# Kernel tuning notes

Hardware: AMD Instinct MI355X
Metric: run time of the kernel (lower is better)

Reference implementation:

```python
import jax, jax.numpy as jnp
import numpy as np

B, L, D_MODEL, H, D_K, D_V = 64, 52, 4096, 32, 128, 128
NEW_C = D_MODEL // H  # per-head input channel after the (faithful) raw reshape


def setup_inputs() -> dict:
    key = jax.random.key(0)
    ks = jax.random.split(key, 12)
    s = 0.02
    return {
        "Q": jax.random.normal(ks[0], (B, L, D_MODEL), jnp.float32),
        "K": jax.random.normal(ks[1], (B, L, D_MODEL), jnp.float32),
        "V": jax.random.normal(ks[2], (B, L, D_MODEL), jnp.float32),
        "Wq": jax.random.normal(ks[3], (H, NEW_C, D_K), jnp.float32) * s,
        "bq": jnp.zeros((H, D_K), jnp.float32),
        "Wk": jax.random.normal(ks[4], (H, NEW_C, D_K), jnp.float32) * s,
        "bk": jnp.zeros((H, D_K), jnp.float32),
        "Wv": jax.random.normal(ks[5], (H, NEW_C, D_V), jnp.float32) * s,
        "bv": jnp.zeros((H, D_V), jnp.float32),
        "Wo": jax.random.normal(ks[6], (H * D_V, D_MODEL), jnp.float32) * s,
        "bo": jnp.zeros((D_MODEL,), jnp.float32),
    }


def reference(Q, K, V, Wq, bq, Wk, bk, Wv, bv, Wo, bo):
    # Faithful to source: raw reshape (B, L, D) -> (B, H, L, D/H), NOT a channel split.
    def split(x):
        return x.reshape(B, H, L, NEW_C)

    q = jnp.einsum('bhlc,hck->bhlk', split(Q), Wq) + bq[None, :, None, :]  # (B,H,L,D_K)
    k = jnp.einsum('bhlc,hck->bhlk', split(K), Wk) + bk[None, :, None, :]
    v = jnp.einsum('bhlc,hcv->bhlv', split(V), Wv) + bv[None, :, None, :]

    scores = jnp.einsum('bhqk,bhmk->bhqm', q, k) / jnp.sqrt(jnp.asarray(D_K, q.dtype))
    # causal mask: keep j <= i, else -inf (matches the numpy masking loop)
    causal = jnp.tril(jnp.ones((L, L), bool))
    scores = jnp.where(causal[None, None], scores, -jnp.inf)
    attn = jax.nn.softmax(scores, axis=-1)
    o = jnp.einsum('bhqm,bhmv->bhqv', attn, v)  # (B,H,L,D_V)
    o = o.transpose(0, 2, 1, 3).reshape(B, L, H * D_V)  # concat heads on last axis
    # Dropout(0.1) is identity at inference.
    return o @ Wo + bo
```

## Files before the change

### kernel.cpp

```cpp
#include <hip/hip_runtime.h>
#include <hip/hip_bf16.h>

#define B_SZ   64
#define L_SZ   52
#define DMODEL 4096
#define H_SZ   32
#define C_SZ   128
#define DK     128

#define GM 3328
#define GN 4096
#define GK 4096

typedef __bf16 bf16x8 __attribute__((ext_vector_type(8)));
typedef float  f32x4  __attribute__((ext_vector_type(4)));

__device__ __forceinline__ void gload_lds16(const void* g, void* l) {
  __builtin_amdgcn_global_load_lds(
      (__attribute__((address_space(1))) void*)(void*)g,
      (__attribute__((address_space(3))) void*)l, 16, 0, 0);
}

__device__ __forceinline__ unsigned short bfbits(float x) {
  union { __hip_bfloat16 h; unsigned short u; } c;
  c.h = __float2bfloat16(x);
  return c.u;
}

__device__ __forceinline__ int hwoff(int row, int g) {
  return row * 128 + ((g ^ (row & 7)) << 3);
}
__device__ __forceinline__ int wdoff(int row, int g) {
  return row * 64 + ((g ^ (row & 7)) << 2);
}

__global__ __launch_bounds__(256) void w3_transpose_kernel(
    const float* __restrict__ Wq, const float* __restrict__ Wk,
    const float* __restrict__ Wv, __hip_bfloat16* __restrict__ WqT,
    __hip_bfloat16* __restrict__ WkT, __hip_bfloat16* __restrict__ WvT) {
  __shared__ float tile[64][65];
  const int bz = blockIdx.z;
  const float* in = (bz < 32 ? Wq : (bz < 64 ? Wk : Wv)) + (size_t)(bz & 31) * 16384;
  __hip_bfloat16* out = (bz < 32 ? WqT : (bz < 64 ? WkT : WvT)) + (size_t)(bz & 31) * 16384;
  const int nt = blockIdx.x, mt = blockIdx.y;
  const int t = threadIdx.x;
  const int r  = t >> 4;
  const int c4 = (t & 15) << 2;
#pragma unroll
  for (int p = 0; p < 4; ++p) {
    const int rr = r + p * 16;
    const float4 v = *(const float4*)(in + (size_t)(mt * 64 + rr) * 128 + nt * 64 + c4);
    tile[rr][c4 + 0] = v.x; tile[rr][c4 + 1] = v.y;
    tile[rr][c4 + 2] = v.z; tile[rr][c4 + 3] = v.w;
  }
  __syncthreads();
#pragma unroll
  for (int p = 0; p < 4; ++p) {
    const int rr = r + p * 16;
    union { __hip_bfloat16 h[4]; ushort4 u; } o4;
#pragma unroll
    for (int e = 0; e < 4; ++e) o4.h[e] = __float2bfloat16(tile[c4 + e][rr]);
    *(ushort4*)(out + (size_t)(nt * 64 + rr) * 128 + mt * 64 + c4) = o4.u;
  }
}

__device__ __forceinline__ void proj_swz(
    const __hip_bfloat16* __restrict__ xs, const __hip_bfloat16* __restrict__ WT,
    const float* __restrict__ bias, __hip_bfloat16* __restrict__ out,
    int n0, int r16, int kq) {
  f32x4 acc[2][4] = {};
  bf16x8 wf[2][4];
#pragma unroll
  for (int ct = 0; ct < 2; ++ct)
#pragma unroll
    for (int kk = 0; kk < 4; ++kk)
      wf[ct][kk] = *(const bf16x8*)(WT + (n0 + ct * 16 + r16) * 128 + kk * 32 + kq * 8);
#pragma unroll
  for (int kk = 0; kk < 4; ++kk) {
    bf16x8 xf[4];
#pragma unroll
    for (int rt = 0; rt < 4; ++rt) {
      const int row = rt * 16 + r16;
      const int rowc = row < 52 ? row : 51;
      xf[rt] = *(const bf16x8*)(xs + hwoff(rowc, 4 * kk + kq));
    }
#pragma unroll
    for (int ct = 0; ct < 2; ++ct)
#pragma unroll
      for (int rt = 0; rt < 4; ++rt)
        acc[ct][rt] = __builtin_amdgcn_mfma_f32_16x16x32_bf16(wf[ct][kk], xf[rt], acc[ct][rt], 0, 0, 0);
  }
#pragma unroll
  for (int ct = 0; ct < 2; ++ct) {
    const int col0 = n0 + ct * 16 + kq * 4;
    const float4 b4 = *(const float4*)(bias + col0);
    const int g = (n0 >> 3) + ct * 2 + (kq >> 1);
#pragma unroll
    for (int rt = 0; rt < 4; ++rt) {
      const int row = rt * 16 + r16;
      if (row < 52) {
        ushort4 o;
        o.x = bfbits(acc[ct][rt][0] + b4.x);
        o.y = bfbits(acc[ct][rt][1] + b4.y);
        o.z = bfbits(acc[ct][rt][2] + b4.z);
        o.w = bfbits(acc[ct][rt][3] + b4.w);
        *(ushort4*)(out + hwoff(row, g) + (kq & 1) * 4) = o;
      }
    }
  }
}

__device__ __forceinline__ uint2 shfl64(uint2 v, int lane) {
  uint2 r;
  r.x = (unsigned)__shfl((int)v.x, lane);
  r.y = (unsigned)__shfl((int)v.y, lane);
  return r;
}

__global__ __launch_bounds__(256, 4) void attn_fused_kernel(
    const float* __restrict__ Qin, const float* __restrict__ Kin,
    const float* __restrict__ Vin,
    const __hip_bfloat16* __restrict__ WqT, const float* __restrict__ bq,
    const __hip_bfloat16* __restrict__ WkT, const float* __restrict__ bk,
    const __hip_bfloat16* __restrict__ WvT, const float* __restrict__ bv,
    __hip_bfloat16* __restrict__ Oc,
    const float* __restrict__ Wo, __hip_bfloat16* __restrict__ WoT) {
  __shared__ __align__(16) char lds[39936];
  const int gid = blockIdx.x;
  const int t = threadIdx.x;

  if (gid >= 2048) {
    float* tile = (float*)lds;
    const int bid2 = gid - 2048;
    const int nt = bid2 & 63, mt = bid2 >> 6;
    const int r  = t >> 4;
    const int c4 = (t & 15) << 2;
#pragma unroll
    for (int p = 0; p < 4; ++p) {
      const int rr = r + p * 16;
      const float4 v = *(const float4*)(Wo + (size_t)(mt * 64 + rr) * 4096 + nt * 64 + c4);
      tile[rr * 65 + c4 + 0] = v.x; tile[rr * 65 + c4 + 1] = v.y;
      tile[rr * 65 + c4 + 2] = v.z; tile[rr * 65 + c4 + 3] = v.w;
    }
    __syncthreads();
#pragma unroll
    for (int p = 0; p < 4; ++p) {
      const int rr = r + p * 16;
      union { __hip_bfloat16 h[4]; ushort4 u; } o4;
#pragma unroll
      for (int e = 0; e < 4; ++e) o4.h[e] = __float2bfloat16(tile[(c4 + e) * 65 + rr]);
      *(ushort4*)(WoT + (size_t)(nt * 64 + rr) * 4096 + mt * 64 + c4) = o4.u;
    }
    return;
  }

  __hip_bfloat16* r0 = (__hip_bfloat16*)(lds);
  __hip_bfloat16* r1 = (__hip_bfloat16*)(lds + 13312);
  __hip_bfloat16* r2 = (__hip_bfloat16*)(lds + 26624);
  float*          s_sh = (float*)(lds + 13312);
  __hip_bfloat16* p_sh = r0;

  const int h = gid & 31, bb = gid >> 5;
  const int lane = t & 63;
  const int w = t >> 6;
  const int r16 = lane & 15, kq = lane >> 4;
  const size_t xoff = (size_t)bb * (L_SZ * DMODEL) + (size_t)h * (L_SZ * C_SZ);
  const int n0 = w * 32;

  {
    const float* xp[3] = {Qin + xoff, Kin + xoff, Vin + xoff};
    __hip_bfloat16* xd[3] = {r0, r1, r2};
#pragma unroll
    for (int tz = 0; tz < 3; ++tz) {
      const float* X = xp[tz];
      __hip_bfloat16* xs = xd[tz];
      for (int idx = t; idx < 52 * 32; idx += 256) {
        const int row = idx >> 5, c4 = (idx & 31) << 2;
        const float4 v = *(const float4*)(X + row * 128 + c4);
        union { __hip_bfloat16 h[4]; ushort4 u; } o4;
        o4.h[0] = __float2bfloat16(v.x); o4.h[1] = __float2bfloat16(v.y);
        o4.h[2] = __float2bfloat16(v.z); o4.h[3] = __float2bfloat16(v.w);
        *(ushort4*)(xs + hwoff(row, c4 >> 3) + (c4 & 4)) = o4.u;
      }
    }
  }
  __syncthreads();

  uint2 vb[4][2];
  {
    f32x4 acc[4][2] = {};
    bf16x8 wf[2][4];
    const __hip_bfloat16* WT = WvT + (size_t)h * 16384;
#pragma unroll
    for (int ct = 0; ct < 2; ++ct)
#pragma unroll
      for (int kk = 0; kk < 4; ++kk)
        wf[ct][kk] = *(const bf16x8*)(WT + (n0 + ct * 16 + r16) * 128 + kk * 32 + kq * 8);
#pragma unroll
    for (int kk = 0; kk < 4; ++kk) {
      bf16x8 a[4];
#pragma unroll
      for (int mt = 0; mt < 4; ++mt) {
        const int row = mt * 16 + r16;
        const int rowc = row < 52 ? row : 51;
        a[mt] = *(const bf16x8*)(r2 + hwoff(rowc, 4 * kk + kq));
      }
#pragma unroll
      for (int mt = 0; mt < 4; ++mt)
#pragma unroll
        for (int ct = 0; ct < 2; ++ct)
          acc[mt][ct] = __builtin_amdgcn_mfma_f32_16x16x32_bf16(a[mt], wf[ct][kk], acc[mt][ct], 0, 0, 0);
    }
#pragma unroll
    for (int ct = 0; ct < 2; ++ct) {
      const float bvv = bv[h * 128 + n0 + ct * 16 + r16];
#pragma unroll
      for (int mt = 0; mt < 4; ++mt) {
        vb[mt][ct].x = (unsigned)bfbits(acc[mt][ct][0] + bvv) |
                       ((unsigned)bfbits(acc[mt][ct][1] + bvv) << 16);
        vb[mt][ct].y = (unsigned)bfbits(acc[mt][ct][2] + bvv) |
                       ((unsigned)bfbits(acc[mt][ct][3] + bvv) << 16);
      }
    }
  }
  __syncthreads();

  proj_swz(r0, WqT + (size_t)h * 16384, bq + h * 128, r2, n0, r16, kq);
  __syncthreads();

  proj_swz(r1, WkT + (size_t)h * 16384, bk + h * 128, r0, n0, r16, kq);
  __syncthreads();

  {
    const int nq = w * 16;
    f32x4 sacc[4] = {};
#pragma unroll
    for (int kk = 0; kk < 4; ++kk) {
      const int krow = nq + r16;
      const int krc = krow < 52 ? krow : 51;
      const bf16x8 kf = *(const bf16x8*)(r0 + hwoff(krc, 4 * kk + kq));
#pragma unroll
      for (int mt = 0; mt < 4; ++mt) {
        const int qrow = mt * 16 + r16;
        const int qrc = qrow < 52 ? qrow : 51;
        const bf16x8 a = *(const bf16x8*)(r2 + hwoff(qrc, 4 * kk + kq));
        sacc[mt] = __builtin_amdgcn_mfma_f32_16x16x32_bf16(a, kf, sacc[mt], 0, 0, 0);
      }
    }
    const float scale = 0.08838834764831845f;
    const int c = nq + r16;
#pragma unroll
    for (int mt = 0; mt < 4; ++mt)
#pragma unroll
      for (int i = 0; i < 4; ++i) {
        const int row = mt * 16 + kq * 4 + i;
        if (row < 52) s_sh[wdoff(row, c >> 2) + (c & 3)] = sacc[mt][i] * scale;
      }
  }
  __syncthreads();

  {
    const int r = t >> 2, qd = t & 3;
    if (r < 52) {
      float v[16];
      float mx = -3e38f;
#pragma unroll
      for (int j4 = 0; j4 < 4; ++j4) {
        const f32x4 s4 = *(const f32x4*)(s_sh + wdoff(r, qd * 4 + j4));
#pragma unroll
        for (int e = 0; e < 4; ++e) {
          const int col = qd * 16 + j4 * 4 + e;
          const float val = (col <= r) ? s4[e] : -3e38f;
          v[j4 * 4 + e] = val;
          mx = fmaxf(mx, val);
        }
      }
      mx = fmaxf(mx, __shfl_xor(mx, 1));
      mx = fmaxf(mx, __shfl_xor(mx, 2));
      float ex[16];
      float sum = 0.f;
#pragma unroll
      for (int j = 0; j < 16; ++j) {
        const int col = qd * 16 + j;
        const float e = (col <= r) ? __expf(v[j] - mx) : 0.f;
        ex[j] = e; sum += e;
      }
      sum += __shfl_xor(sum, 1);
      sum += __shfl_xor(sum, 2);
      const float inv = 1.0f / sum;
      union { __hip_bfloat16 h[8]; uint4 q; } p0, p1;
#pragma unroll
      for (int j = 0; j < 8; ++j) {
        p0.h[j] = __float2bfloat16(ex[j] * inv);
        p1.h[j] = __float2bfloat16(ex[8 + j] * inv);
      }
      *(uint4*)(p_sh + hwoff(r, qd * 2))     = p0.q;
      *(uint4*)(p_sh + hwoff(r, qd * 2 + 1)) = p1.q;
    }
  }
  __syncthreads();

  {
    const int half = (kq >> 1) & 1;
    const int src0 = ((kq & 1) << 5) + r16;
    const int src1 = src0 + 16;
    f32x4 oaccT[2][4] = {};
#pragma unroll
    for (int kk = 0; kk < 2; ++kk) {
      bf16x8 bfr[2];
#pragma unroll
      for (int ct = 0; ct < 2; ++ct) {
        const uint2 a0 = shfl64(vb[2 * kk + 0][ct], src0);
        const uint2 a1 = shfl64(vb[2 * kk + 1][ct], src0);
        const uint2 b0 = shfl64(vb[2 * kk + 0][ct], src1);
        const uint2 b1 = shfl64(vb[2 * kk + 1][ct], src1);
        union { unsigned u[4]; bf16x8 v; } asm_;
        asm_.u[0] = half ? a1.x : a0.x;
        asm_.u[1] = half ? a1.y : a0.y;
        asm_.u[2] = half ? b1.x : b0.x;
        asm_.u[3] = half ? b1.y : b0.y;
        bfr[ct] = asm_.v;
      }
      bf16x8 pf[4];
#pragma unroll
      for (int rt = 0; rt < 4; ++rt) {
        const int prow = rt * 16 + r16;
        const int prc = prow < 52 ? prow : 51;
        pf[rt] = *(const bf16x8*)(p_sh + hwoff(prc, 4 * kk + kq));
      }
#pragma unroll
      for (int ct = 0; ct < 2; ++ct)
#pragma unroll
        for (int rt = 0; rt < 4; ++rt)
          oaccT[ct][rt] = __builtin_amdgcn_mfma_f32_16x16x32_bf16(bfr[ct], pf[rt], oaccT[ct][rt], 0, 0, 0);
    }
    const size_t obase = (size_t)bb * 52 * 4096 + (size_t)h * 128;
#pragma unroll
    for (int ct = 0; ct < 2; ++ct) {
      const int col0 = n0 + ct * 16 + kq * 4;
#pragma unroll
      for (int rt = 0; rt < 4; ++rt) {
        const int row = rt * 16 + r16;
        if (row < 52) {
          ushort4 o;
          o.x = bfbits(oaccT[ct][rt][0]);
          o.y = bfbits(oaccT[ct][rt][1]);
          o.z = bfbits(oaccT[ct][rt][2]);
          o.w = bfbits(oaccT[ct][rt][3]);
          *(ushort4*)(Oc + obase + (size_t)row * 4096 + col0) = o;
        }
      }
    }
  }
}

#define STAGE(GBASE, REGOFF, KT, KS, WB) do {                                  \
    const __hip_bfloat16* s_ = (GBASE) + (size_t)(KT) * 64 + (KS) * 32;        \
    char* d_ = (WB) + (REGOFF) + ((KS) ? 16384 : 0) + t * 16;                  \
    gload_lds16(s_, d_);                                                       \
    gload_lds16(s_ + (size_t)128 * GK, d_ + 8192);                             \
  } while (0)

#define MFMA16(MQ, BF)                                                         \
  __builtin_amdgcn_sched_barrier(0);                                           \
  __builtin_amdgcn_s_setprio(1);                                               \
  _Pragma("unroll")                                                            \
  for (int mf = 0; mf < 4; ++mf)                                               \
    _Pragma("unroll")                                                          \
    for (int nf = 0; nf < 4; ++nf)                                             \
      acc[(MQ) * 4 + mf][nf] = __builtin_amdgcn_mfma_f32_16x16x32_bf16(        \
          af[mf], BF[nf], acc[(MQ) * 4 + mf][nf], 0, 0, 0);                    \
  __builtin_amdgcn_s_setprio(0)

#define READ_AF(RB, KS, MQ)                                                    \
  _Pragma("unroll")                                                            \
  for (int mf = 0; mf < 4; ++mf)                                               \
    af[mf] = *(const bf16x8*)((RB) + (KS) * 16384 + (MQ) * 4096 + aB0 + mf * 1024)

#define READ_BF(RB, BF, KS)                                                    \
  _Pragma("unroll")                                                            \
  for (int nf = 0; nf < 4; ++nf)                                               \
    BF[nf] = *(const bf16x8*)((RB) + 32768 + (KS) * 16384 + bB0 + nf * 1024)

#define KTILE_BODY(KT, RB, OB) do {                                            \
    const int s1 = (KT) + 1 < 64 ? (KT) + 1 : 63;                              \
    const int s2 = (KT) + 2 < 64 ? (KT) + 2 : 63;                              \
    {                                                                          \
      bf16x8 af[4];                                                            \
      READ_AF(RB, 0, 0);                                                       \
      READ_BF(RB, bf0, 0);                                                     \
      STAGE(gA0, 0, s1, 1, OB);                                                \
      __builtin_amdgcn_s_barrier();                                            \
      asm volatile("s_waitcnt lgkmcnt(0)" ::: "memory");                       \
      MFMA16(0, bf0);                                                          \
      __builtin_amdgcn_s_barrier();                                            \
    }                                                                          \
    {                                                                          \
      bf16x8 af[4];                                                            \
      READ_AF(RB, 0, 1);                                                       \
      STAGE(gB0, 32768, s2, 0, RB);                                            \
      __builtin_amdgcn_s_barrier();                                            \
      asm volatile("s_waitcnt lgkmcnt(0)" ::: "memory");                       \
      MFMA16(1, bf0);                                                          \
      __builtin_amdgcn_s_barrier();                                            \
    }                                                                          \
    {                                                                          \
      bf16x8 af[4];                                                            \
      READ_AF(RB, 1, 0);                                                       \
      READ_BF(RB, bf1, 1);                                                     \
      STAGE(gA0, 0, s2, 0, RB);                                                \
      __builtin_amdgcn_s_barrier();                                            \
      asm volatile("s_waitcnt lgkmcnt(0)" ::: "memory");                       \
      MFMA16(0, bf1);                                                          \
      __builtin_amdgcn_s_barrier();                                            \
    }                                                                          \
    {                                                                          \
      bf16x8 af[4];                                                            \
      READ_AF(RB, 1, 1);                                                       \
      STAGE(gB0, 32768, s2, 1, RB);                                            \
      __builtin_amdgcn_s_barrier();                                            \
      asm volatile("s_waitcnt lgkmcnt(0)" ::: "memory");                       \
      MFMA16(1, bf1);                                                          \
      asm volatile("s_waitcnt vmcnt(6)" ::: "memory");                         \
      __builtin_amdgcn_s_barrier();                                            \
    }                                                                          \
  } while (0)

__global__ __launch_bounds__(512, 2) void out_gemm_kernel(
    const __hip_bfloat16* __restrict__ A, const __hip_bfloat16* __restrict__ Bt,
    const float* __restrict__ bias, float* __restrict__ C) {
  __shared__ __align__(16) char lds[131072];

  int bid = blockIdx.x;
  bid = (bid & 7) * 26 + (bid >> 3);
  const int tm = bid >> 4;
  const int tn = bid & 15;

  const int t = threadIdx.x;
  const int w = t >> 6, lane = t & 63;
  const int wm = w >> 2, wn = w & 3;
  const int r16 = lane & 15, kq = lane >> 4;

  const int srow = t >> 2;
  const int sgslot = (t & 3) ^ ((srow >> 1) & 3);
  const __hip_bfloat16* gA0 = A  + (size_t)(tm * 256 + srow) * GK + sgslot * 8;
  const __hip_bfloat16* gB0 = Bt + (size_t)(tn * 256 + srow) * GK + sgslot * 8;

  const int slotr = kq ^ ((r16 >> 1) & 3);
  const int aB0 = (wm * 128 + r16) * 64 + slotr * 16;
  const int bB0 = (wn * 64 + r16) * 64 + slotr * 16;

  f32x4 acc[8][4] = {};
  bf16x8 bf0[4], bf1[4];

  char* const buf0 = lds;
  char* const buf1 = lds + 65536;

  STAGE(gA0, 0,     0, 0, buf0);
  STAGE(gA0, 0,     0, 1, buf0);
  STAGE(gB0, 32768, 0, 0, buf0);
  STAGE(gB0, 32768, 0, 1, buf0);
  STAGE(gB0, 32768, 1, 0, buf1);
  STAGE(gA0, 0,     1, 0, buf1);
  STAGE(gB0, 32768, 1, 1, buf1);
  asm volatile("s_waitcnt vmcnt(6)" ::: "memory");
  __builtin_amdgcn_s_barrier();

#pragma unroll 1
  for (int kt2 = 0; kt2 < 32; ++kt2) {
    const int kt = kt2 * 2;
    KTILE_BODY(kt,     buf0, buf1);
    KTILE_BODY(kt + 1, buf1, buf0);
  }
  asm volatile("s_waitcnt vmcnt(0) lgkmcnt(0)" ::: "memory");

  const int row0 = tm * 256 + wm * 128 + kq * 4;
  const int col0 = tn * 256 + wn * 64 + r16;
#pragma unroll
  for (int nf = 0; nf < 4; ++nf) {
    const int col = col0 + nf * 16;
    const float bv = bias[col];
#pragma unroll
    for (int mf = 0; mf < 8; ++mf) {
      const int row = row0 + mf * 16;
#pragma unroll
      for (int i = 0; i < 4; ++i)
        C[(size_t)(row + i) * GN + col] = acc[mf][nf][i] + bv;
    }
  }
}

extern "C" void kernel_launch(void* const* d_in, const int* in_sizes, int n_in,
                              void* d_out, int out_size, void* d_ws, size_t ws_size,
                              hipStream_t stream) {
  const float* Q  = (const float*)d_in[0];
  const float* K  = (const float*)d_in[1];
  const float* V  = (const float*)d_in[2];
  const float* Wq = (const float*)d_in[3];
  const float* bq = (const float*)d_in[4];
  const float* Wk = (const float*)d_in[5];
  const float* bk = (const float*)d_in[6];
  const float* Wv = (const float*)d_in[7];
  const float* bv = (const float*)d_in[8];
  const float* Wo = (const float*)d_in[9];
  const float* bo = (const float*)d_in[10];
  float* out = (float*)d_out;

  char* wsb = (char*)d_ws;
  __hip_bfloat16* WoT = (__hip_bfloat16*)wsb;
  __hip_bfloat16* Oc  = (__hip_bfloat16*)(wsb + (size_t)GN * GK * 2);
  __hip_bfloat16* WqT = (__hip_bfloat16*)(wsb + (size_t)GN * GK * 2 + (size_t)GM * GN * 2);
  __hip_bfloat16* WkT = WqT + (size_t)H_SZ * C_SZ * DK;
  __hip_bfloat16* WvT = WkT + (size_t)H_SZ * C_SZ * DK;

  w3_transpose_kernel<<<dim3(2, 2, 96), 256, 0, stream>>>(Wq, Wk, Wv, WqT, WkT, WvT);
  attn_fused_kernel<<<dim3(2048 + 4096), 256, 0, stream>>>(
      Q, K, V, WqT, bq, WkT, bk, WvT, bv, Oc, Wo, WoT);
  out_gemm_kernel<<<dim3(13 * 16), 512, 0, stream>>>(Oc, WoT, bo, out);
}
```

Measured before the change: 196.5 us.

## Pad LDS rows instead of XOR swizzle, batch input loads, vectorize GEMM epilogue

```diff
diff --git a/kernel.cpp b/kernel.cpp
--- a/kernel.cpp
+++ b/kernel.cpp
@@ -25,13 +25,6 @@
   union { __hip_bfloat16 h; unsigned short u; } c;
   c.h = __float2bfloat16(x);
   return c.u;
-}
-
-__device__ __forceinline__ int hwoff(int row, int g) {
-  return row * 128 + ((g ^ (row & 7)) << 3);
-}
-__device__ __forceinline__ int wdoff(int row, int g) {
-  return row * 64 + ((g ^ (row & 7)) << 2);
 }
 
 __global__ __launch_bounds__(256) void w3_transpose_kernel(
@@ -64,7 +57,7 @@
   }
 }
 
-__device__ __forceinline__ void proj_swz(
+__device__ __forceinline__ void proj_swap136(
     const __hip_bfloat16* __restrict__ xs, const __hip_bfloat16* __restrict__ WT,
     const float* __restrict__ bias, __hip_bfloat16* __restrict__ out,
     int n0, int r16, int kq) {
@@ -82,7 +75,7 @@
     for (int rt = 0; rt < 4; ++rt) {
       const int row = rt * 16 + r16;
       const int rowc = row < 52 ? row : 51;
-      xf[rt] = *(const bf16x8*)(xs + hwoff(rowc, 4 * kk + kq));
+      xf[rt] = *(const bf16x8*)(xs + rowc * 136 + kk * 32 + kq * 8);
     }
 #pragma unroll
     for (int ct = 0; ct < 2; ++ct)
@@ -94,7 +87,6 @@
   for (int ct = 0; ct < 2; ++ct) {
     const int col0 = n0 + ct * 16 + kq * 4;
     const float4 b4 = *(const float4*)(bias + col0);
-    const int g = (n0 >> 3) + ct * 2 + (kq >> 1);
 #pragma unroll
     for (int rt = 0; rt < 4; ++rt) {
       const int row = rt * 16 + r16;
@@ -104,7 +96,7 @@
         o.y = bfbits(acc[ct][rt][1] + b4.y);
         o.z = bfbits(acc[ct][rt][2] + b4.z);
         o.w = bfbits(acc[ct][rt][3] + b4.w);
-        *(ushort4*)(out + hwoff(row, g) + (kq & 1) * 4) = o;
+        *(ushort4*)(out + row * 136 + col0) = o;
       }
     }
   }
@@ -117,7 +109,7 @@
   return r;
 }
 
-__global__ __launch_bounds__(256, 4) void attn_fused_kernel(
+__global__ __launch_bounds__(256, 3) void attn_fused_kernel(
     const float* __restrict__ Qin, const float* __restrict__ Kin,
     const float* __restrict__ Vin,
     const __hip_bfloat16* __restrict__ WqT, const float* __restrict__ bq,
@@ -125,7 +117,7 @@
     const __hip_bfloat16* __restrict__ WvT, const float* __restrict__ bv,
     __hip_bfloat16* __restrict__ Oc,
     const float* __restrict__ Wo, __hip_bfloat16* __restrict__ WoT) {
-  __shared__ __align__(16) char lds[39936];
+  __shared__ __align__(16) char lds[42432];
   const int gid = blockIdx.x;
   const int t = threadIdx.x;
 
@@ -155,9 +147,9 @@
   }
 
   __hip_bfloat16* r0 = (__hip_bfloat16*)(lds);
-  __hip_bfloat16* r1 = (__hip_bfloat16*)(lds + 13312);
-  __hip_bfloat16* r2 = (__hip_bfloat16*)(lds + 26624);
-  float*          s_sh = (float*)(lds + 13312);
+  __hip_bfloat16* r1 = (__hip_bfloat16*)(lds + 14144);
+  __hip_bfloat16* r2 = (__hip_bfloat16*)(lds + 28288);
+  float*          s_sh = (float*)(lds + 14144);
   __hip_bfloat16* p_sh = r0;
 
   const int h = gid & 31, bb = gid >> 5;
@@ -167,35 +159,45 @@
   const size_t xoff = (size_t)bb * (L_SZ * DMODEL) + (size_t)h * (L_SZ * C_SZ);
   const int n0 = w * 32;
 
+#define LOADR(G, XP)                                                           \
+  _Pragma("unroll")                                                            \
+  for (int j = 0; j < 7; ++j) {                                                \
+    const int idx = t + j * 256;                                               \
+    if (idx < 1664)                                                            \
+      G[j] = *(const float4*)((XP) + (idx >> 5) * 128 + ((idx & 31) << 2));    \
+  }
+#define STORER(G, XD)                                                          \
+  _Pragma("unroll")                                                            \
+  for (int j = 0; j < 7; ++j) {                                                \
+    const int idx = t + j * 256;                                               \
+    if (idx < 1664) {                                                          \
+      ushort4 o;                                                               \
+      o.x = bfbits(G[j].x); o.y = bfbits(G[j].y);                              \
+      o.z = bfbits(G[j].z); o.w = bfbits(G[j].w);                              \
+      *(ushort4*)((XD) + (idx >> 5) * 136 + ((idx & 31) << 2)) = o;            \
+    }                                                                          \
+  }
+  bf16x8 wfv[2][4];
   {
-    const float* xp[3] = {Qin + xoff, Kin + xoff, Vin + xoff};
-    __hip_bfloat16* xd[3] = {r0, r1, r2};
-#pragma unroll
-    for (int tz = 0; tz < 3; ++tz) {
-      const float* X = xp[tz];
-      __hip_bfloat16* xs = xd[tz];
-      for (int idx = t; idx < 52 * 32; idx += 256) {
-        const int row = idx >> 5, c4 = (idx & 31) << 2;
-        const float4 v = *(const float4*)(X + row * 128 + c4);
-        union { __hip_bfloat16 h[4]; ushort4 u; } o4;
-        o4.h[0] = __float2bfloat16(v.x); o4.h[1] = __float2bfloat16(v.y);
-        o4.h[2] = __float2bfloat16(v.z); o4.h[3] = __float2bfloat16(v.w);
-        *(ushort4*)(xs + hwoff(row, c4 >> 3) + (c4 & 4)) = o4.u;
-      }
-    }
+    float4 ga[7], gb[7];
+    LOADR(ga, Qin + xoff)
+    LOADR(gb, Kin + xoff)
+    const __hip_bfloat16* WTv = WvT + (size_t)h * 16384;
+#pragma unroll
+    for (int ct = 0; ct < 2; ++ct)
+#pragma unroll
+      for (int kk = 0; kk < 4; ++kk)
+        wfv[ct][kk] = *(const bf16x8*)(WTv + (n0 + ct * 16 + r16) * 128 + kk * 32 + kq * 8);
+    STORER(ga, r0)
+    LOADR(ga, Vin + xoff)
+    STORER(gb, r1)
+    STORER(ga, r2)
   }
   __syncthreads();
 
   uint2 vb[4][2];
   {
     f32x4 acc[4][2] = {};
-    bf16x8 wf[2][4];
-    const __hip_bfloat16* WT = WvT + (size_t)h * 16384;
-#pragma unroll
-    for (int ct = 0; ct < 2; ++ct)
-#pragma unroll
-      for (int kk = 0; kk < 4; ++kk)
-        wf[ct][kk] = *(const bf16x8*)(WT + (n0 + ct * 16 + r16) * 128 + kk * 32 + kq * 8);
 #pragma unroll
     for (int kk = 0; kk < 4; ++kk) {
       bf16x8 a[4];
@@ -203,13 +205,13 @@
       for (int mt = 0; mt < 4; ++mt) {
         const int row = mt * 16 + r16;
         const int rowc = row < 52 ? row : 51;
-        a[mt] = *(const bf16x8*)(r2 + hwoff(rowc, 4 * kk + kq));
+        a[mt] = *(const bf16x8*)(r2 + rowc * 136 + kk * 32 + kq * 8);
       }
 #pragma unroll
       for (int mt = 0; mt < 4; ++mt)
 #pragma unroll
         for (int ct = 0; ct < 2; ++ct)
-          acc[mt][ct] = __builtin_amdgcn_mfma_f32_16x16x32_bf16(a[mt], wf[ct][kk], acc[mt][ct], 0, 0, 0);
+          acc[mt][ct] = __builtin_amdgcn_mfma_f32_16x16x32_bf16(a[mt], wfv[ct][kk], acc[mt][ct], 0, 0, 0);
     }
 #pragma unroll
     for (int ct = 0; ct < 2; ++ct) {
@@ -225,10 +227,10 @@
   }
   __syncthreads();
 
-  proj_swz(r0, WqT + (size_t)h * 16384, bq + h * 128, r2, n0, r16, kq);
-  __syncthreads();
-
-  proj_swz(r1, WkT + (size_t)h * 16384, bk + h * 128, r0, n0, r16, kq);
+  proj_swap136(r0, WqT + (size_t)h * 16384, bq + h * 128, r2, n0, r16, kq);
+  __syncthreads();
+
+  proj_swap136(r1, WkT + (size_t)h * 16384, bk + h * 128, r0, n0, r16, kq);
   __syncthreads();
 
   {
@@ -238,23 +240,22 @@
     for (int kk = 0; kk < 4; ++kk) {
       const int krow = nq + r16;
       const int krc = krow < 52 ? krow : 51;
-      const bf16x8 kf = *(const bf16x8*)(r0 + hwoff(krc, 4 * kk + kq));
+      const bf16x8 kf = *(const bf16x8*)(r0 + krc * 136 + kk * 32 + kq * 8);
 #pragma unroll
       for (int mt = 0; mt < 4; ++mt) {
         const int qrow = mt * 16 + r16;
         const int qrc = qrow < 52 ? qrow : 51;
-        const bf16x8 a = *(const bf16x8*)(r2 + hwoff(qrc, 4 * kk + kq));
+        const bf16x8 a = *(const bf16x8*)(r2 + qrc * 136 + kk * 32 + kq * 8);
         sacc[mt] = __builtin_amdgcn_mfma_f32_16x16x32_bf16(a, kf, sacc[mt], 0, 0, 0);
       }
     }
     const float scale = 0.08838834764831845f;
-    const int c = nq + r16;
 #pragma unroll
     for (int mt = 0; mt < 4; ++mt)
 #pragma unroll
       for (int i = 0; i < 4; ++i) {
         const int row = mt * 16 + kq * 4 + i;
-        if (row < 52) s_sh[wdoff(row, c >> 2) + (c & 3)] = sacc[mt][i] * scale;
+        if (row < 52) s_sh[row * 68 + nq + r16] = sacc[mt][i] * scale;
       }
   }
   __syncthreads();
@@ -266,7 +267,7 @@
       float mx = -3e38f;
 #pragma unroll
       for (int j4 = 0; j4 < 4; ++j4) {
-        const f32x4 s4 = *(const f32x4*)(s_sh + wdoff(r, qd * 4 + j4));
+        const f32x4 s4 = *(const f32x4*)(s_sh + r * 68 + qd * 16 + j4 * 4);
 #pragma unroll
         for (int e = 0; e < 4; ++e) {
           const int col = qd * 16 + j4 * 4 + e;
@@ -294,8 +295,8 @@
         p0.h[j] = __float2bfloat16(ex[j] * inv);
         p1.h[j] = __float2bfloat16(ex[8 + j] * inv);
       }
-      *(uint4*)(p_sh + hwoff(r, qd * 2))     = p0.q;
-      *(uint4*)(p_sh + hwoff(r, qd * 2 + 1)) = p1.q;
+      *(uint4*)(p_sh + r * 72 + qd * 16)     = p0.q;
+      *(uint4*)(p_sh + r * 72 + qd * 16 + 8) = p1.q;
     }
   }
   __syncthreads();
@@ -326,7 +327,7 @@
       for (int rt = 0; rt < 4; ++rt) {
         const int prow = rt * 16 + r16;
         const int prc = prow < 52 ? prow : 51;
-        pf[rt] = *(const bf16x8*)(p_sh + hwoff(prc, 4 * kk + kq));
+        pf[rt] = *(const bf16x8*)(p_sh + prc * 72 + kk * 32 + kq * 8);
       }
 #pragma unroll
       for (int ct = 0; ct < 2; ++ct)
@@ -369,7 +370,7 @@
     _Pragma("unroll")                                                          \
     for (int nf = 0; nf < 4; ++nf)                                             \
       acc[(MQ) * 4 + mf][nf] = __builtin_amdgcn_mfma_f32_16x16x32_bf16(        \
-          af[mf], BF[nf], acc[(MQ) * 4 + mf][nf], 0, 0, 0);                    \
+          BF[nf], af[mf], acc[(MQ) * 4 + mf][nf], 0, 0, 0);                    \
   __builtin_amdgcn_s_setprio(0)
 
 #define READ_AF(RB, KS, MQ)                                                    \
@@ -474,18 +475,23 @@
   }
   asm volatile("s_waitcnt vmcnt(0) lgkmcnt(0)" ::: "memory");
 
-  const int row0 = tm * 256 + wm * 128 + kq * 4;
-  const int col0 = tn * 256 + wn * 64 + r16;
-#pragma unroll
-  for (int nf = 0; nf < 4; ++nf) {
-    const int col = col0 + nf * 16;
-    const float bv = bias[col];
-#pragma unroll
-    for (int mf = 0; mf < 8; ++mf) {
-      const int row = row0 + mf * 16;
-#pragma unroll
-      for (int i = 0; i < 4; ++i)
-        C[(size_t)(row + i) * GN + col] = acc[mf][nf][i] + bv;
+  const int row0 = tm * 256 + wm * 128 + r16;
+  const int col0 = tn * 256 + wn * 64 + kq * 4;
+  float4 b4[4];
+#pragma unroll
+  for (int nf = 0; nf < 4; ++nf)
+    b4[nf] = *(const float4*)(bias + col0 + nf * 16);
+#pragma unroll
+  for (int mf = 0; mf < 8; ++mf) {
+    const int row = row0 + mf * 16;
+#pragma unroll
+    for (int nf = 0; nf < 4; ++nf) {
+      float4 st;
+      st.x = acc[mf][nf][0] + b4[nf].x;
+      st.y = acc[mf][nf][1] + b4[nf].y;
+      st.z = acc[mf][nf][2] + b4[nf].z;
+      st.w = acc[mf][nf][3] + b4[nf].w;
+      *(float4*)(C + (size_t)row * GN + col0 + nf * 16) = st;
     }
   }
 }
```

Result: faster. 185.6 us (-5.6%).
